# Optimization experiments

Measured on AMD Instinct MI355X. Metric: run time of the kernel, lower is better.

## Reference

```python
import jax, jax.numpy as jnp
import numpy as np

N_NODES = 20000
N_EDGES = 320000
N_GRAPHS = 64
F_IN = 128
HID = 512


def gcn_conv(x, edge_index, W, b):
    """PyG GCNConv: x' = D^{-1/2} (A + I) D^{-1/2} (x W) + b."""
    n = x.shape[0]
    h = x @ W  # [N, out]
    loop = jnp.arange(n, dtype=edge_index.dtype)
    src = jnp.concatenate([edge_index[0], loop])  # sources (message senders)
    dst = jnp.concatenate([edge_index[1], loop])  # targets (aggregation)
    deg = jnp.zeros((n,), dtype=h.dtype).at[dst].add(1.0)
    dinv = jnp.where(deg > 0, jax.lax.rsqrt(deg), 0.0)
    norm = dinv[src] * dinv[dst]  # [E+N]
    msg = h[src] * norm[:, None]  # gather + scale
    out = jax.ops.segment_sum(msg, dst, num_segments=n)
    return out + b


def global_mean_pool(x, batch, num_graphs):
    s = jax.ops.segment_sum(x, batch, num_segments=num_graphs)
    cnt = jax.ops.segment_sum(jnp.ones((x.shape[0],), dtype=x.dtype), batch, num_segments=num_graphs)
    return s / jnp.clip(cnt, 1.0)[:, None]


def setup_inputs() -> dict:
    key = jax.random.key(0)
    ks = jax.random.split(key, 12)
    x = jax.random.normal(ks[0], (N_NODES, F_IN), dtype=jnp.float32)
    edge_index = jax.random.randint(ks[1], (2, N_EDGES), 0, N_NODES, dtype=jnp.int64 if jax.config.jax_enable_x64 else jnp.int32)
    batch = jnp.sort(jax.random.randint(ks[2], (N_NODES,), 0, N_GRAPHS, dtype=edge_index.dtype))

    def glorot(k, fan_in, fan_out):
        lim = float(np.sqrt(6.0 / (fan_in + fan_out)))
        return jax.random.uniform(k, (fan_in, fan_out), jnp.float32, -lim, lim)

    W1 = glorot(ks[3], F_IN, HID)
    b1 = jnp.zeros((HID,), jnp.float32)
    W2 = glorot(ks[4], HID, HID // 2)
    b2 = jnp.zeros((HID // 2,), jnp.float32)
    W3 = glorot(ks[5], HID // 2, HID // 4)
    b3 = jnp.zeros((HID // 4,), jnp.float32)
    Wl = glorot(ks[6], HID // 4, 2)
    bl = jnp.zeros((2,), jnp.float32)
    return {"x": x, "edge_index": edge_index, "batch": batch,
            "W1": W1, "b1": b1, "W2": W2, "b2": b2,
            "W3": W3, "b3": b3, "Wl": Wl, "bl": bl}


def reference(x, edge_index, batch, W1, b1, W2, b2, W3, b3, Wl, bl):
    h = jax.nn.relu(gcn_conv(x, edge_index, W1, b1))
    h = jax.nn.relu(gcn_conv(h, edge_index, W2, b2))
    h = gcn_conv(h, edge_index, W3, b3)
    g = global_mean_pool(h, batch, N_GRAPHS)  # [G, HID//4]
    # dropout p=0.5 is identity in eval mode
    return g @ Wl + bl  # [G, 2]
```

## Files before the change

### kernel.cpp

```cpp
#include <hip/hip_runtime.h>
#include <hip/hip_bf16.h>


#define N_NODES_C  20000
#define N_GRAPHS_C 64
#define HID_C      512

typedef __attribute__((ext_vector_type(8))) _Float16 f16x8;
typedef __attribute__((ext_vector_type(8))) unsigned short u16x8;
typedef __attribute__((ext_vector_type(4))) float f32x4;

static __device__ __forceinline__ unsigned short f2h(float f) {
    _Float16 h = (_Float16)f;
    return __builtin_bit_cast(unsigned short, h);
}
static __device__ __forceinline__ float h2f(unsigned short u) {
    return (float)__builtin_bit_cast(_Float16, u);
}
static __device__ __forceinline__ float hu_lo(unsigned u) {
    return (float)__builtin_bit_cast(_Float16, (unsigned short)(u & 0xffffu));
}
static __device__ __forceinline__ float hu_hi(unsigned u) {
    return (float)__builtin_bit_cast(_Float16, (unsigned short)(u >> 16));
}

__global__ __launch_bounds__(1024) void scan_kernel(const int* __restrict__ deg_cnt,
                                                    int* __restrict__ row_ptr,
                                                    int* __restrict__ cursor,
                                                    float* __restrict__ dinv, int n) {
    __shared__ int ws[16];
    int t = threadIdx.x;
    int wid = t >> 6, lane = t & 63;
    int carry = 0;
    for (int base = 0; base < n; base += 1024) {
        int idx = base + t;
        int v = (idx < n) ? deg_cnt[idx] : 0;
        int x = v;
        #pragma unroll
        for (int off = 1; off < 64; off <<= 1) {
            int y = __shfl_up(x, off);
            if (lane >= off) x += y;
        }
        if (lane == 63) ws[wid] = x;
        __syncthreads();
        if (wid == 0 && lane < 16) {
            int w = ws[lane];
            #pragma unroll
            for (int off = 1; off < 16; off <<= 1) {
                int y = __shfl_up(w, off);
                if (lane >= off) w += y;
            }
            ws[lane] = w;
        }
        __syncthreads();
        int wave_excl = (wid == 0) ? 0 : ws[wid - 1];
        int total = ws[15];
        if (idx < n) {
            int rp = carry + wave_excl + (x - v);
            row_ptr[idx] = rp;
            cursor[idx]  = rp;
            dinv[idx]    = rsqrtf((float)(v + 1));
        }
        carry += total;
        __syncthreads();
    }
    if (t == 0) row_ptr[n] = carry;
}

static __device__ __forceinline__ void wconv_body(const float* __restrict__ W, int i,
                                                  int Kd, int Nd,
                                                  unsigned short* __restrict__ WT) {
    int k = i / Nd, n = i % Nd;
    WT[(size_t)n * Kd + k] = f2h(W[i]);
}

__global__ void prep_kernel(const int* __restrict__ dst, int* __restrict__ deg_cnt, int E,
                            const float* __restrict__ W1, const float* __restrict__ W2,
                            const float* __restrict__ W3,
                            unsigned short* __restrict__ W1T,
                            unsigned short* __restrict__ W2T,
                            unsigned short* __restrict__ W3T,
                            const int* __restrict__ batch, int n, int ngraphs,
                            int* __restrict__ gstart) {
    int t = blockIdx.x * blockDim.x + threadIdx.x;
    if (t < E) {
        atomicAdd(&deg_cnt[dst[t]], 1);
        return;
    }
    t -= E;
    if (t < 128 * 512) { wconv_body(W1, t, 128, 512, W1T); return; }
    t -= 128 * 512;
    if (t < 512 * 256) { wconv_body(W2, t, 512, 256, W2T); return; }
    t -= 512 * 256;
    if (t < 256 * 128) { wconv_body(W3, t, 256, 128, W3T); return; }
    t -= 256 * 128;
    {
        int i = t;
        if (i >= n) return;
        int b = batch[i];
        if (i == 0) {
            for (int g = 0; g <= b; ++g) gstart[g] = 0;
        } else {
            int bp = batch[i - 1];
            if (bp != b) for (int g = bp + 1; g <= b; ++g) gstart[g] = i;
        }
        if (i == n - 1) {
            for (int g = b + 1; g <= ngraphs; ++g) gstart[g] = n;
        }
    }
}

__global__ void fillx_kernel(const int* __restrict__ src, const int* __restrict__ dst,
                             int* __restrict__ cursor, int* __restrict__ col_idx, int E,
                             const float* __restrict__ x, const float* __restrict__ dinv,
                             unsigned short* __restrict__ xs, int nrows) {
    int t = blockIdx.x * blockDim.x + threadIdx.x;
    if (t < E) {
        int d = dst[t];
        int pos = atomicAdd(&cursor[d], 1);
        col_idx[pos] = src[t];
    } else {
        int u = t - E;
        int row = u >> 5, q = u & 31;
        if (row >= nrows) return;
        float di = dinv[row];
        f32x4 v = *reinterpret_cast<const f32x4*>(&x[(size_t)row * 128 + q * 4]);
        ushort4 o;
        o.x = f2h(v.x * di); o.y = f2h(v.y * di);
        o.z = f2h(v.z * di); o.w = f2h(v.w * di);
        *reinterpret_cast<ushort4*>(&xs[(size_t)row * 128 + q * 4]) = o;
    }
}

template <int F, bool BIAS, bool RELU>
__global__ __launch_bounds__(256) void agg_kernel(const unsigned short* __restrict__ hs,
                                                  const float* __restrict__ dinv,
                                                  const int* __restrict__ row_ptr,
                                                  const int* __restrict__ col_idx,
                                                  const float* __restrict__ bias,
                                                  unsigned short* __restrict__ out, int n) {
    constexpr int CPL = F / 32;
    __shared__ float red[3 * F];
    int i = blockIdx.x;
    int tid = threadIdx.x;
    int wid = tid >> 6, lane = tid & 63;
    int h = lane >> 5, l32 = lane & 31;
    int e0 = row_ptr[i], e1 = row_ptr[i + 1];
    int deg = e1 - e0;

    float acc[CPL];
    #pragma unroll
    for (int v = 0; v < CPL; ++v) acc[v] = 0.f;

    if (wid == 0 && h == 0) {
        const unsigned short* p = &hs[(size_t)i * F + l32 * CPL];
        if constexpr (CPL == 4) {
            uint2 u = *reinterpret_cast<const uint2*>(p);
            acc[0] = hu_lo(u.x); acc[1] = hu_hi(u.x);
            acc[2] = hu_lo(u.y); acc[3] = hu_hi(u.y);
        } else {
            uint4 u = *reinterpret_cast<const uint4*>(p);
            acc[0] = hu_lo(u.x); acc[1] = hu_hi(u.x);
            acc[2] = hu_lo(u.y); acc[3] = hu_hi(u.y);
            acc[4] = hu_lo(u.z); acc[5] = hu_hi(u.z);
            acc[6] = hu_lo(u.w); acc[7] = hu_hi(u.w);
        }
    }

    int per = (deg + 3) >> 2;
    int cs = e0 + wid * per;
    int ce = cs + per; if (ce > e1) ce = e1;
    for (int base = cs; base < ce; base += 64) {
        int rem = ce - base;
        int mm = rem < 64 ? rem : 64;
        int myidx = col_idx[base + (lane < mm ? lane : 0)];
        for (int p0 = 0; 2 * p0 < mm; p0 += 4) {
            #pragma unroll
            for (int k = 0; k < 4; ++k) {
                int j = 2 * (p0 + k) + h;
                int jc = j < mm ? j : 0;
                int srcn = __shfl(myidx, jc);
                float w = (j < mm) ? 1.f : 0.f;
                const unsigned short* p = &hs[(size_t)srcn * F + l32 * CPL];
                if constexpr (CPL == 4) {
                    uint2 u = *reinterpret_cast<const uint2*>(p);
                    acc[0] = fmaf(hu_lo(u.x), w, acc[0]);
                    acc[1] = fmaf(hu_hi(u.x), w, acc[1]);
                    acc[2] = fmaf(hu_lo(u.y), w, acc[2]);
                    acc[3] = fmaf(hu_hi(u.y), w, acc[3]);
                } else {
                    uint4 u = *reinterpret_cast<const uint4*>(p);
                    acc[0] = fmaf(hu_lo(u.x), w, acc[0]);
                    acc[1] = fmaf(hu_hi(u.x), w, acc[1]);
                    acc[2] = fmaf(hu_lo(u.y), w, acc[2]);
                    acc[3] = fmaf(hu_hi(u.y), w, acc[3]);
                    acc[4] = fmaf(hu_lo(u.z), w, acc[4]);
                    acc[5] = fmaf(hu_hi(u.z), w, acc[5]);
                    acc[6] = fmaf(hu_lo(u.w), w, acc[6]);
                    acc[7] = fmaf(hu_hi(u.w), w, acc[7]);
                }
            }
        }
    }

    #pragma unroll
    for (int v = 0; v < CPL; ++v) acc[v] += __shfl_xor(acc[v], 32);

    if (wid > 0 && h == 0) {
        float* r = &red[(wid - 1) * F + l32 * CPL];
        #pragma unroll
        for (int v = 0; v < CPL; v += 4)
            *reinterpret_cast<float4*>(&r[v]) = make_float4(acc[v], acc[v+1], acc[v+2], acc[v+3]);
    }
    __syncthreads();
    if (wid == 0 && h == 0) {
        #pragma unroll
        for (int w = 0; w < 3; ++w)
            #pragma unroll
            for (int v = 0; v < CPL; ++v) acc[v] += red[w * F + l32 * CPL + v];
        float di = dinv[i];
        unsigned short ov[CPL];
        #pragma unroll
        for (int v = 0; v < CPL; ++v) {
            float r = di * acc[v];
            if (BIAS) r += bias[l32 * CPL + v];
            if (RELU) r = fmaxf(r, 0.f);
            ov[v] = f2h(r);
        }
        if constexpr (CPL == 4) {
            uint2 o;
            o.x = (unsigned)ov[0] | ((unsigned)ov[1] << 16);
            o.y = (unsigned)ov[2] | ((unsigned)ov[3] << 16);
            *reinterpret_cast<uint2*>(&out[(size_t)i * F + l32 * CPL]) = o;
        } else {
            uint4 o;
            o.x = (unsigned)ov[0] | ((unsigned)ov[1] << 16);
            o.y = (unsigned)ov[2] | ((unsigned)ov[3] << 16);
            o.z = (unsigned)ov[4] | ((unsigned)ov[5] << 16);
            o.w = (unsigned)ov[6] | ((unsigned)ov[7] << 16);
            *reinterpret_cast<uint4*>(&out[(size_t)i * F + l32 * CPL]) = o;
        }
    }
}

template <int K, int N, int BM, int BN, bool BIAS, bool RELU, bool SCALE>
__global__ __launch_bounds__(256) void gemm_mfma(const unsigned short* __restrict__ A,
                                                 const unsigned short* __restrict__ WT,
                                                 const float* __restrict__ bias,
                                                 const float* __restrict__ dinvp,
                                                 unsigned short* __restrict__ C, int M) {
    constexpr int BK = 64;
    constexpr int MI = BM / 32;
    constexpr int WN = BN / 32;
    __shared__ unsigned short As[BM * BK];
    __shared__ unsigned short Bs[BN * BK];

    const int tid = threadIdx.x;
    const int wid = tid >> 6;
    const int lane16 = tid & 15;
    const int quad = (tid >> 4) & 3;
    const int wm = (wid >> 1) * (BM / 2);
    const int wn = (wid & 1) * (BN / 2);
    const int bm = blockIdx.x * BM;
    const int bn = blockIdx.y * BN;

    f32x4 acc[MI][WN];
    #pragma unroll
    for (int mi = 0; mi < MI; ++mi)
        #pragma unroll
        for (int ni = 0; ni < WN; ++ni) acc[mi][ni] = (f32x4)(0.f);

    for (int kt = 0; kt < K / BK; ++kt) {
        #pragma unroll
        for (int c = 0; c < (BM * 8) / 256; ++c) {
            int ch = tid + c * 256;
            int row = ch >> 3, kc = ch & 7;
            int gm = bm + row;
            u16x8 av = (u16x8)(0);
            if (gm < M) av = *reinterpret_cast<const u16x8*>(&A[(size_t)gm * K + kt * BK + kc * 8]);
            *reinterpret_cast<u16x8*>(&As[row * 64 + ((kc * 8) ^ ((row & 7) << 3))]) = av;
        }
        #pragma unroll
        for (int c = 0; c < (BN * 8) / 256; ++c) {
            int ch = tid + c * 256;
            int row = ch >> 3, kc = ch & 7;
            u16x8 bv = *reinterpret_cast<const u16x8*>(&WT[(size_t)(bn + row) * K + kt * BK + kc * 8]);
            *reinterpret_cast<u16x8*>(&Bs[row * 64 + ((kc * 8) ^ ((row & 7) << 3))]) = bv;
        }
        __syncthreads();

        #pragma unroll
        for (int ks = 0; ks < 2; ++ks) {
            f16x8 af[MI], bf[WN];
            #pragma unroll
            for (int mi = 0; mi < MI; ++mi) {
                int row = wm + mi * 16 + lane16;
                int kidx = ks * 32 + quad * 8;
                af[mi] = *reinterpret_cast<f16x8*>(&As[row * 64 + (kidx ^ ((row & 7) << 3))]);
            }
            #pragma unroll
            for (int ni = 0; ni < WN; ++ni) {
                int row = wn + ni * 16 + lane16;
                int kidx = ks * 32 + quad * 8;
                bf[ni] = *reinterpret_cast<f16x8*>(&Bs[row * 64 + (kidx ^ ((row & 7) << 3))]);
            }
            #pragma unroll
            for (int mi = 0; mi < MI; ++mi)
                #pragma unroll
                for (int ni = 0; ni < WN; ++ni)
                    acc[mi][ni] = __builtin_amdgcn_mfma_f32_16x16x32_f16(af[mi], bf[ni], acc[mi][ni], 0, 0, 0);
        }
        __syncthreads();
    }

    #pragma unroll
    for (int mi = 0; mi < MI; ++mi) {
        #pragma unroll
        for (int r = 0; r < 4; ++r) {
            int gm = bm + wm + mi * 16 + quad * 4 + r;
            if (gm >= M) continue;
            float sc = SCALE ? dinvp[gm] : 1.f;
            #pragma unroll
            for (int ni = 0; ni < WN; ++ni) {
                int gn = bn + wn + ni * 16 + lane16;
                float v = acc[mi][ni][r];
                if (BIAS) v += bias[gn];
                if (RELU) v = fmaxf(v, 0.f);
                if (SCALE) v *= sc;
                C[(size_t)gm * N + gn] = f2h(v);
            }
        }
    }
}

__global__ void pool_partial_kernel(const unsigned short* __restrict__ A,
                                    const int* __restrict__ gstart,
                                    float* __restrict__ partial) {
    __shared__ float sd[256];
    int g = blockIdx.x, y = blockIdx.y;
    int t = threadIdx.x;
    int c = t & 127, r = t >> 7;
    int s0 = gstart[g], s1 = gstart[g + 1];
    float s = 0.f;
    for (int i = s0 + y * 2 + r; i < s1; i += 16)
        s += h2f(A[(size_t)i * 128 + c]);
    sd[t] = s;
    __syncthreads();
    if (t < 128) partial[(size_t)(g * 8 + y) * 128 + c] = sd[t] + sd[t + 128];
}

__global__ void poolfinal_kernel(const float* __restrict__ partial,
                                 const int* __restrict__ gstart,
                                 const float* __restrict__ Wl, const float* __restrict__ bl,
                                 float* __restrict__ out) {
    __shared__ float2 red[128];
    int g = blockIdx.x, c = threadIdx.x;
    float s = 0.f;
    #pragma unroll
    for (int y = 0; y < 8; ++y) s += partial[(size_t)(g * 8 + y) * 128 + c];
    int cnt = gstart[g + 1] - gstart[g];
    if (cnt < 1) cnt = 1;
    float p = s / (float)cnt;
    red[c] = make_float2(p * Wl[c * 2 + 0], p * Wl[c * 2 + 1]);
    __syncthreads();
    for (int off = 64; off > 0; off >>= 1) {
        if (c < off) {
            red[c].x += red[c + off].x;
            red[c].y += red[c + off].y;
        }
        __syncthreads();
    }
    if (c == 0) {
        out[g * 2 + 0] = red[0].x + bl[0];
        out[g * 2 + 1] = red[0].y + bl[1];
    }
}

extern "C" void kernel_launch(void* const* d_in, const int* in_sizes, int n_in,
                              void* d_out, int out_size, void* d_ws, size_t ws_size,
                              hipStream_t stream) {
    const float* x   = (const float*)d_in[0];
    const int*   ei  = (const int*)d_in[1];
    const int*   bat = (const int*)d_in[2];
    const float* W1  = (const float*)d_in[3];
    const float* b1  = (const float*)d_in[4];
    const float* W2  = (const float*)d_in[5];
    const float* b2  = (const float*)d_in[6];
    const float* W3  = (const float*)d_in[7];
    const float* b3  = (const float*)d_in[8];
    const float* Wl  = (const float*)d_in[9];
    const float* bl  = (const float*)d_in[10];
    float* out = (float*)d_out;

    const int N = N_NODES_C;
    const int E = in_sizes[1] / 2;
    const int G = N_GRAPHS_C;

    const int* src = ei;
    const int* dst = ei + E;

    unsigned short* xs  = (unsigned short*)d_ws;
    unsigned short* A1b = xs  + (size_t)N * 128;
    unsigned short* H1  = A1b + (size_t)N * 128;
    unsigned short* T2s = H1  + (size_t)N * 512;
    unsigned short* H2  = T2s + (size_t)N * 256;
    unsigned short* T3s = H2  + (size_t)N * 256;
    unsigned short* A3  = T3s + (size_t)N * 128;
    unsigned short* W1T = A3  + (size_t)N * 128;
    unsigned short* W2T = W1T + 512 * 128;
    unsigned short* W3T = W2T + 256 * 512;
    int*   deg_cnt = (int*)(W3T + 128 * 256);
    int*   row_ptr = deg_cnt + N;
    int*   cursor  = row_ptr + (N + 1);
    int*   col_idx = cursor + N;
    float* dinv    = (float*)(col_idx + E);
    int*   gstart  = (int*)(dinv + N);
    float* partial = (float*)(gstart + (G + 4));

    hipMemsetAsync(deg_cnt, 0, N * sizeof(int), stream);
    {
        int total = E + 128 * 512 + 512 * 256 + 256 * 128 + N;
        prep_kernel<<<(total + 255) / 256, 256, 0, stream>>>(dst, deg_cnt, E,
                                                             W1, W2, W3, W1T, W2T, W3T,
                                                             bat, N, G, gstart);
    }
    scan_kernel<<<1, 1024, 0, stream>>>(deg_cnt, row_ptr, cursor, dinv, N);
    {
        int total = E + N * 32;
        fillx_kernel<<<(total + 255) / 256, 256, 0, stream>>>(src, dst, cursor, col_idx, E,
                                                              x, dinv, xs, N);
    }

    const int MB128 = (N + 127) / 128;
    const int MB64  = (N + 63) / 64;

    agg_kernel<128, false, false><<<N, 256, 0, stream>>>(xs, dinv, row_ptr, col_idx, nullptr, A1b, N);
    {
        dim3 grid(MB128, 512 / 128);
        gemm_mfma<128, 512, 128, 128, true, true, false><<<grid, 256, 0, stream>>>(A1b, W1T, b1, nullptr, H1, N);
    }
    {
        dim3 grid(MB64, 256 / 128);
        gemm_mfma<512, 256, 64, 128, false, false, true><<<grid, 256, 0, stream>>>(H1, W2T, nullptr, dinv, T2s, N);
    }
    agg_kernel<256, true, true><<<N, 256, 0, stream>>>(T2s, dinv, row_ptr, col_idx, b2, H2, N);
    {
        dim3 grid(MB64, 128 / 64);
        gemm_mfma<256, 128, 64, 64, false, false, true><<<grid, 256, 0, stream>>>(H2, W3T, nullptr, dinv, T3s, N);
    }
    agg_kernel<128, true, false><<<N, 256, 0, stream>>>(T3s, dinv, row_ptr, col_idx, b3, A3, N);

    {
        dim3 grid(G, 8);
        pool_partial_kernel<<<grid, 256, 0, stream>>>(A3, gstart, partial);
    }
    poolfinal_kernel<<<G, 128, 0, stream>>>(partial, gstart, Wl, bl, out);
}
```

Baseline: 177.7 us.

## Parallelize degree scan per wave, deepen gather unroll, shrink layer-1 GEMM tile

The single-block scan now splits the nodes into 16 contiguous wave ranges. It sums each range first, then each wave scans its own range independently, which removes the per-chunk block barriers. The aggregation gather loop unrolls 8 neighbor pairs instead of 4 to keep more loads in flight. The first GEMM uses 64-row tiles instead of 128, doubling the block count for better occupancy, at some cost in weight reuse.

```diff
diff --git a/kernel.cpp b/kernel.cpp
--- a/kernel.cpp
+++ b/kernel.cpp
@@ -31,40 +31,43 @@
     __shared__ int ws[16];
     int t = threadIdx.x;
     int wid = t >> 6, lane = t & 63;
+    const int RANGE = (n + 15) >> 4;
+    const int ROUNDS = (RANGE + 63) >> 6;
+    int base = wid * RANGE;
+
+    int s = 0;
+    for (int r = 0; r < ROUNDS; ++r) {
+        int off = r * 64 + lane;
+        int idx = base + off;
+        if (off < RANGE && idx < n) s += deg_cnt[idx];
+    }
+    #pragma unroll
+    for (int o = 32; o > 0; o >>= 1) s += __shfl_xor(s, o);
+    if (lane == 0) ws[wid] = s;
+    __syncthreads();
+
     int carry = 0;
-    for (int base = 0; base < n; base += 1024) {
-        int idx = base + t;
-        int v = (idx < n) ? deg_cnt[idx] : 0;
+    for (int j = 0; j < wid; ++j) carry += ws[j];
+
+    for (int r = 0; r < ROUNDS; ++r) {
+        int off = r * 64 + lane;
+        int idx = base + off;
+        int v = (off < RANGE && idx < n) ? deg_cnt[idx] : 0;
         int x = v;
         #pragma unroll
-        for (int off = 1; off < 64; off <<= 1) {
-            int y = __shfl_up(x, off);
-            if (lane >= off) x += y;
-        }
-        if (lane == 63) ws[wid] = x;
-        __syncthreads();
-        if (wid == 0 && lane < 16) {
-            int w = ws[lane];
-            #pragma unroll
-            for (int off = 1; off < 16; off <<= 1) {
-                int y = __shfl_up(w, off);
-                if (lane >= off) w += y;
-            }
-            ws[lane] = w;
-        }
-        __syncthreads();
-        int wave_excl = (wid == 0) ? 0 : ws[wid - 1];
-        int total = ws[15];
-        if (idx < n) {
-            int rp = carry + wave_excl + (x - v);
+        for (int o = 1; o < 64; o <<= 1) {
+            int y = __shfl_up(x, o);
+            if (lane >= o) x += y;
+        }
+        if (off < RANGE && idx < n) {
+            int rp = carry + x - v;
             row_ptr[idx] = rp;
             cursor[idx]  = rp;
             dinv[idx]    = rsqrtf((float)(v + 1));
         }
-        carry += total;
-        __syncthreads();
-    }
-    if (t == 0) row_ptr[n] = carry;
+        carry += __shfl(x, 63);
+    }
+    if (t == 1023) row_ptr[n] = carry;
 }
 
 static __device__ __forceinline__ void wconv_body(const float* __restrict__ W, int i,
@@ -174,9 +177,9 @@
         int rem = ce - base;
         int mm = rem < 64 ? rem : 64;
         int myidx = col_idx[base + (lane < mm ? lane : 0)];
-        for (int p0 = 0; 2 * p0 < mm; p0 += 4) {
-            #pragma unroll
-            for (int k = 0; k < 4; ++k) {
+        for (int p0 = 0; 2 * p0 < mm; p0 += 8) {
+            #pragma unroll
+            for (int k = 0; k < 8; ++k) {
                 int j = 2 * (p0 + k) + h;
                 int jc = j < mm ? j : 0;
                 int srcn = __shfl(myidx, jc);
@@ -431,13 +434,12 @@
                                                               x, dinv, xs, N);
     }
 
-    const int MB128 = (N + 127) / 128;
-    const int MB64  = (N + 63) / 64;
+    const int MB64 = (N + 63) / 64;
 
     agg_kernel<128, false, false><<<N, 256, 0, stream>>>(xs, dinv, row_ptr, col_idx, nullptr, A1b, N);
     {
-        dim3 grid(MB128, 512 / 128);
-        gemm_mfma<128, 512, 128, 128, true, true, false><<<grid, 256, 0, stream>>>(A1b, W1T, b1, nullptr, H1, N);
+        dim3 grid(MB64, 512 / 128);
+        gemm_mfma<128, 512, 64, 128, true, true, false><<<grid, 256, 0, stream>>>(A1b, W1T, b1, nullptr, H1, N);
     }
     {
         dim3 grid(MB64, 256 / 128);
```

Result: slower. 212.7 us (+19.7%).
